# Kernel optimization log

Measured on AMD Instinct MI355X. Metric: run time of the kernel, lower is better.

## Reference

```python
import jax, jax.numpy as jnp
import numpy as np

B, T, H, L, AS = 64, 256, 1024, 3, 128  # batch, seq-1, hidden, layers, alphabet


def setup_inputs() -> dict:
    key = jax.random.key(0)
    ks = jax.random.split(key, 8)
    # one-hot character sequence (B, T, AS), float32
    idx = jax.random.randint(ks[0], (B, T), 0, AS)
    sequence = jax.nn.one_hot(idx, AS, dtype=jnp.float32)
    u = lambda k, shape, fan: jax.random.uniform(
        k, shape, minval=-1.0 / np.sqrt(fan), maxval=1.0 / np.sqrt(fan), dtype=jnp.float32)
    W_i2h = u(ks[1], (H, AS), AS)
    b_i2h = u(ks[2], (H,), AS)
    # per-layer LSTM params, PyTorch gate order [i, f, g, o]; layer inputs all have width H
    W_ih = u(ks[3], (L, 4 * H, H), H)
    W_hh = u(ks[4], (L, 4 * H, H), H)
    b_ih = u(ks[5], (L, 4 * H), H)
    b_hh = u(ks[6], (L, 4 * H), H)
    W_h2O = u(ks[7], (AS, H), H)
    b_h2O = jnp.zeros((AS,), dtype=jnp.float32)
    h0 = jnp.zeros((L, B, H), dtype=jnp.float32)
    c0 = jnp.zeros((L, B, H), dtype=jnp.float32)
    return dict(sequence=sequence, W_i2h=W_i2h, b_i2h=b_i2h, W_ih=W_ih, W_hh=W_hh,
                b_ih=b_ih, b_hh=b_hh, W_h2O=W_h2O, b_h2O=b_h2O, h0=h0, c0=c0)


def _lstm_layer(x, h0, c0, W_ih, W_hh, b_ih, b_hh):
    # x: (B, T, H). Precompute input contribution to the gates for all steps.
    xg = jnp.einsum('bth,gh->btg', x, W_ih) + b_ih  # (B, T, 4H)

    def step(carry, xg_t):
        h, c = carry
        gates = xg_t + h @ W_hh.T + b_hh  # (B, 4H)
        i, f, g, o = jnp.split(gates, 4, axis=-1)
        c = jax.nn.sigmoid(f) * c + jax.nn.sigmoid(i) * jnp.tanh(g)
        h = jax.nn.sigmoid(o) * jnp.tanh(c)
        return (h, c), h

    (hT, cT), hs = jax.lax.scan(step, (h0, c0), jnp.swapaxes(xg, 0, 1))
    return jnp.swapaxes(hs, 0, 1), hT, cT  # (B,T,H), (B,H), (B,H)


def reference(sequence, W_i2h, b_i2h, W_ih, W_hh, b_ih, b_hh, W_h2O, b_h2O, h0, c0):
    # i2h projection
    x = jnp.einsum('bta,ha->bth', sequence, W_i2h) + b_i2h  # (B, T, H)
    # multi-layer LSTM over x (eval mode: the dropout=True arg is inactive in eval)
    inp = x
    h_fin, c_fin = [], []
    for l in range(L):
        inp, hT, cT = _lstm_layer(inp, h0[l], c0[l], W_ih[l], W_hh[l], b_ih[l], b_hh[l])
        h_fin.append(hT)
        c_fin.append(cT)
    # NOTE: faithful to the original code's bug -- h2O is applied to the i2h
    # output `x`, not to the LSTM output. The LSTM only produces the new hidden.
    out = x.reshape(-1, H) @ W_h2O.T + b_h2O  # (B*T, AS)
    return out, jnp.stack(h_fin), jnp.stack(c_fin)
```

## Files before the change

### kernel.cpp

```cpp
#include <hip/hip_runtime.h>
#include <stdint.h>
#include <stddef.h>

#define B_  64
#define T_  256
#define H_  1024
#define AS_ 128
#define L_  3

typedef __attribute__((ext_vector_type(8))) short bf16x8;
typedef __attribute__((ext_vector_type(4))) float f32x4;
typedef __attribute__((ext_vector_type(4))) unsigned u32x4;

__device__ __forceinline__ unsigned short f2bf(float f) {
  union { float f; unsigned u; } x; x.f = f;
  unsigned r = x.u + 0x7fffu + ((x.u >> 16) & 1u);
  return (unsigned short)(r >> 16);
}
__device__ __forceinline__ float bf2f(unsigned short s) {
  union { unsigned u; float f; } x; x.u = ((unsigned)s) << 16; return x.f;
}
__device__ __forceinline__ float sigmf(float x) { return 1.0f / (1.0f + __expf(-x)); }
__device__ __forceinline__ float tanh_f(float x) {
  x = fminf(fmaxf(x, -15.0f), 15.0f);
  float e = __expf(2.0f * x);
  return (e - 1.0f) / (e + 1.0f);
}

__device__ __forceinline__ void st_u16_cc(unsigned short* p, unsigned short v) {
  __hip_atomic_store(p, v, __ATOMIC_RELAXED, __HIP_MEMORY_SCOPE_AGENT);
}
__device__ __forceinline__ void st_u32_cc(unsigned* p, unsigned v) {
  __hip_atomic_store(p, v, __ATOMIC_RELAXED, __HIP_MEMORY_SCOPE_AGENT);
}
__device__ __forceinline__ unsigned ld_u32_cc(const unsigned* p) {
  return __hip_atomic_load(p, __ATOMIC_RELAXED, __HIP_MEMORY_SCOPE_AGENT);
}
__device__ __forceinline__ u32x4 ld_b128_cc_nw(const void* p) {
  u32x4 r;
  asm volatile("global_load_dwordx4 %0, %1, off sc0 sc1" : "=v"(r) : "v"(p));
  return r;
}
__device__ __forceinline__ void wait_vm4_tie4(u32x4& a, u32x4& b, u32x4& c, u32x4& d) {
  asm volatile("s_waitcnt vmcnt(4)"
               : "+v"(a), "+v"(b), "+v"(c), "+v"(d) :: "memory");
  __builtin_amdgcn_sched_barrier(0);
}
__device__ __forceinline__ void wait_vm0_tie4(u32x4& a, u32x4& b, u32x4& c, u32x4& d) {
  asm volatile("s_waitcnt vmcnt(0)"
               : "+v"(a), "+v"(b), "+v"(c), "+v"(d) :: "memory");
  __builtin_amdgcn_sched_barrier(0);
}
__device__ __forceinline__ void lds_barrier() {
  __builtin_amdgcn_sched_barrier(0);
  asm volatile("s_waitcnt lgkmcnt(0)" ::: "memory");
  __builtin_amdgcn_sched_barrier(0);
  __builtin_amdgcn_s_barrier();
  __builtin_amdgcn_sched_barrier(0);
}


__global__ void k_zero(unsigned* p, int n) {
  int i = blockIdx.x * 256 + threadIdx.x;
  if (i < n) st_u32_cc(p + i, 0u);
}

__global__ void k_wt_i2h(const float* __restrict__ W, const float* __restrict__ b,
                         unsigned short* __restrict__ Wt) {
  int id = blockIdx.x * 256 + threadIdx.x;
  if (id >= AS_ * H_) return;
  int a = id >> 10, h = id & 1023;
  Wt[id] = f2bf(W[h * AS_ + a] + b[h]);
}

__global__ void k_f2b(const float* __restrict__ s, unsigned short* __restrict__ d, int n) {
  int i = blockIdx.x * 256 + threadIdx.x;
  if (i < n) d[i] = f2bf(s[i]);
}

__global__ void k_bias(const float* __restrict__ bi, const float* __restrict__ bh,
                       float* __restrict__ o, int n) {
  int i = blockIdx.x * 256 + threadIdx.x;
  if (i < n) o[i] = bi[i] + bh[i];
}

__global__ __launch_bounds__(128) void k_gather(const float* __restrict__ seq,
                                                const unsigned short* __restrict__ Wt,
                                                unsigned short* __restrict__ xbf) {
  __shared__ int sidx;
  const int bt = blockIdx.x, tid = threadIdx.x;
  if (seq[(size_t)bt * AS_ + tid] > 0.5f) sidx = tid;
  __syncthreads();
  const uint4* s = (const uint4*)(Wt + (size_t)sidx * H_);
  uint4* d = (uint4*)(xbf + (size_t)bt * H_);
  d[tid] = s[tid];
}


__device__ __forceinline__ void gld16(const void* g, void* l) {
  __builtin_amdgcn_global_load_lds((const __attribute__((address_space(1))) unsigned int*)g,
                                   (__attribute__((address_space(3))) unsigned int*)l,
                                   16, 0, 0);
}

template <int OUT>
__global__ __launch_bounds__(256) void k_gemm(const unsigned short* __restrict__ A,
                                              const unsigned short* __restrict__ Bm,
                                              const float* __restrict__ bias,
                                              void* __restrict__ Cout,
                                              int M, int N, int K) {
  __shared__ __align__(16) unsigned short As[128 * 32];
  __shared__ __align__(16) unsigned short Bs[128 * 32];
  const int tid = threadIdx.x, lane = tid & 63, wv = tid >> 6;
  const int m0 = blockIdx.x * 128, n0 = blockIdx.y * 128;
  const int wr = wv >> 1, wc = wv & 1;
  const int kg = lane >> 4, li = lane & 15;
  f32x4 acc[4][4] = {};

  for (int k0 = 0; k0 < K; k0 += 32) {
    for (int i = 0; i < 2; ++i) {
      int c0 = i * 256 + wv * 64;
      int cid = c0 + lane;
      int row = cid >> 2, lc = cid & 3;
      int sc = lc ^ ((row >> 1) & 3);
      gld16(A + (size_t)(m0 + row) * K + k0 + sc * 8, (char*)As + (size_t)c0 * 16);
      gld16(Bm + (size_t)(n0 + row) * K + k0 + sc * 8, (char*)Bs + (size_t)c0 * 16);
    }
    __syncthreads();
    bf16x8 af[4], bfm[4];
#pragma unroll
    for (int mi = 0; mi < 4; ++mi) {
      int row = wr * 64 + mi * 16 + li;
      int pc = kg ^ ((row >> 1) & 3);
      af[mi] = *(const bf16x8*)((const char*)As + row * 64 + pc * 16);
    }
#pragma unroll
    for (int ni = 0; ni < 4; ++ni) {
      int row = wc * 64 + ni * 16 + li;
      int pc = kg ^ ((row >> 1) & 3);
      bfm[ni] = *(const bf16x8*)((const char*)Bs + row * 64 + pc * 16);
    }
#pragma unroll
    for (int mi = 0; mi < 4; ++mi)
#pragma unroll
      for (int ni = 0; ni < 4; ++ni)
        acc[mi][ni] = __builtin_amdgcn_mfma_f32_16x16x32_bf16(af[mi], bfm[ni], acc[mi][ni], 0, 0, 0);
    __syncthreads();
  }

#pragma unroll
  for (int mi = 0; mi < 4; ++mi)
#pragma unroll
    for (int ni = 0; ni < 4; ++ni)
#pragma unroll
      for (int r = 0; r < 4; ++r) {
        int row = m0 + wr * 64 + mi * 16 + kg * 4 + r;
        int col = n0 + wc * 64 + ni * 16 + li;
        float v = acc[mi][ni][r] + bias[col];
        if (OUT == 0) {
          ((float*)Cout)[(size_t)row * N + col] = v;
        } else {
          int b = row >> 8, tt = row & 255;
          int g = col >> 10, u = col & 1023;
          int idx = ((tt * 4 + (b >> 4)) << 16) | ((u >> 5) << 11) |
                    ((b & 15) << 7) | ((u & 31) << 2) | g;
          ((unsigned short*)Cout)[idx] = f2bf(v);
        }
      }
}


__global__ __launch_bounds__(256, 1) void k_scan(
    const unsigned short* __restrict__ xgs,
    const float* __restrict__ Whh,
    unsigned short* __restrict__ h_pp,
    unsigned short* __restrict__ out_seq,
    float* __restrict__ hT, float* __restrict__ cT,
    const float* __restrict__ h0, const float* __restrict__ c0,
    unsigned* __restrict__ slots) {
  __shared__ __align__(16) unsigned short Wlds[64 * 1024];
  __shared__ __align__(16) unsigned short Hs[16 * 1024];
  const int tid = threadIdx.x, lane = tid & 63, w = tid >> 6;
  const int gb = blockIdx.x >> 5, ug = blockIdx.x & 31;
  const int li = lane & 15, kq = lane >> 4;
  const int b  = gb * 16 + li;
  const int u0 = ug * 32 + w * 8 + kq;
  const int u1 = u0 + 4;

  st_u16_cc(&h_pp[((size_t)B_ + b) * H_ + u0], f2bf(h0[(size_t)b * H_ + u0]));
  st_u16_cc(&h_pp[((size_t)B_ + b) * H_ + u1], f2bf(h0[(size_t)b * H_ + u1]));

  bf16x8 afr[32];
  {
    const int r0 = w * 32 + li;
    const float* wr = Whh + ((size_t)(r0 & 3) * H_ + ug * 32 + (r0 >> 2)) * H_ + kq * 8;
#pragma unroll
    for (int ks = 0; ks < 32; ++ks) {
      const float4 f0 = *(const float4*)(wr + ks * 32);
      const float4 f1 = *(const float4*)(wr + ks * 32 + 4);
      union { ushort4 a[2]; bf16x8 v; } uu_;
      uu_.a[0] = ushort4{f2bf(f0.x), f2bf(f0.y), f2bf(f0.z), f2bf(f0.w)};
      uu_.a[1] = ushort4{f2bf(f1.x), f2bf(f1.y), f2bf(f1.z), f2bf(f1.w)};
      afr[ks] = uu_.v;
    }
  }
  for (int it = 0; it < 16; ++it) {
    const int r = w * 32 + 16 + it;
    const float* wr = Whh + ((size_t)(r & 3) * H_ + ug * 32 + (r >> 2)) * H_;
#pragma unroll
    for (int j = 0; j < 4; ++j) {
      const float4 f = *(const float4*)(wr + lane * 16 + j * 4);
      ushort4 p = ushort4{f2bf(f.x), f2bf(f.y), f2bf(f.z), f2bf(f.w)};
      const int k = lane * 16 + j * 4;
      *(ushort4*)((char*)Wlds + (size_t)(w * 16 + it) * 2048 + ((2 * k) ^ ((it & 7) << 4))) = p;
    }
  }
  float cs0 = c0[(size_t)b * H_ + u0], cs1 = c0[(size_t)b * H_ + u1];
  __syncthreads();
  if (w == 3 && lane < 32) {
    st_u32_cc(&slots[gb * 1024 + lane * 32 + ug], 1u);
    asm volatile("s_waitcnt vmcnt(0)" ::: "memory");
  }

  const char* hbase = (const char*)Hs + (size_t)li * 2048;
  const char* wlb   = (const char*)Wlds + (size_t)(w * 16 + li) * 2048;
  const int fxor = (li & 7) << 4;
  const int sb = tid >> 4, seg = tid & 15;
  const int sswz = (sb & 7) << 4;
  char* drow = (char*)Hs + (size_t)sb * 2048;
  unsigned short* exch = Hs;
  const unsigned* myline = slots + gb * 1024 + ug * 32;

  for (int t = 0; t < T_; ++t) {
    const size_t xb2 = ((((size_t)t * 4 + gb) << 16) | (ug << 11) | (li << 7) |
                        ((w * 8 + kq) << 2)) * 2;
    const ushort4 xa = *(const ushort4*)((const char*)xgs + xb2);
    const ushort4 xb = *(const ushort4*)((const char*)xgs + xb2 + 32);

    if (w == 0) {
      const unsigned tgt = (unsigned)(t + 1);
      unsigned v;
      do {
        __builtin_amdgcn_s_sleep(1);
        v = ld_u32_cc(&myline[lane & 31]);
      } while (__any((int)(v < tgt)));
    }
    __syncthreads();

    const char* srcrow = (const char*)(h_pp + (size_t)((t & 1) ^ 1) * (B_ * H_) +
                                       (size_t)(gb * 16 + sb) * H_);
    u32x4 A0 = ld_b128_cc_nw(srcrow +   0 * 256 + seg * 16);
    u32x4 A1 = ld_b128_cc_nw(srcrow +   1 * 256 + seg * 16);
    u32x4 A2 = ld_b128_cc_nw(srcrow +   2 * 256 + seg * 16);
    u32x4 A3 = ld_b128_cc_nw(srcrow +   3 * 256 + seg * 16);
    u32x4 B0 = ld_b128_cc_nw(srcrow + 1024 + 0 * 256 + seg * 16);
    u32x4 B1 = ld_b128_cc_nw(srcrow + 1024 + 1 * 256 + seg * 16);
    u32x4 B2 = ld_b128_cc_nw(srcrow + 1024 + 2 * 256 + seg * 16);
    u32x4 B3 = ld_b128_cc_nw(srcrow + 1024 + 3 * 256 + seg * 16);
    wait_vm4_tie4(A0, A1, A2, A3);
    *(u32x4*)(drow + ((0 * 256 + seg * 16) ^ sswz)) = A0;
    *(u32x4*)(drow + ((1 * 256 + seg * 16) ^ sswz)) = A1;
    *(u32x4*)(drow + ((2 * 256 + seg * 16) ^ sswz)) = A2;
    *(u32x4*)(drow + ((3 * 256 + seg * 16) ^ sswz)) = A3;
    lds_barrier();

    f32x4 a0 = {0.f, 0.f, 0.f, 0.f}, a1 = {0.f, 0.f, 0.f, 0.f};
#pragma unroll
    for (int ks = 0; ks < 16; ++ks) {
      const bf16x8 bb = *(const bf16x8*)(hbase + ((ks * 64 + kq * 16) ^ fxor));
      a0 = __builtin_amdgcn_mfma_f32_16x16x32_bf16(afr[ks], bb, a0, 0, 0, 0);
      const bf16x8 aw = *(const bf16x8*)(wlb + ((ks * 64 + kq * 16) ^ fxor));
      a1 = __builtin_amdgcn_mfma_f32_16x16x32_bf16(aw, bb, a1, 0, 0, 0);
    }

    wait_vm0_tie4(B0, B1, B2, B3);
    *(u32x4*)(drow + ((1024 + 0 * 256 + seg * 16) ^ sswz)) = B0;
    *(u32x4*)(drow + ((1024 + 1 * 256 + seg * 16) ^ sswz)) = B1;
    *(u32x4*)(drow + ((1024 + 2 * 256 + seg * 16) ^ sswz)) = B2;
    *(u32x4*)(drow + ((1024 + 3 * 256 + seg * 16) ^ sswz)) = B3;
    lds_barrier();

#pragma unroll
    for (int ks = 16; ks < 32; ++ks) {
      const bf16x8 bb = *(const bf16x8*)(hbase + ((ks * 64 + kq * 16) ^ fxor));
      a0 = __builtin_amdgcn_mfma_f32_16x16x32_bf16(afr[ks], bb, a0, 0, 0, 0);
      const bf16x8 aw = *(const bf16x8*)(wlb + ((ks * 64 + kq * 16) ^ fxor));
      a1 = __builtin_amdgcn_mfma_f32_16x16x32_bf16(aw, bb, a1, 0, 0, 0);
    }

    float h0v, h1v;
    {
      float gi = a0[0] + bf2f(xa.x), gf = a0[1] + bf2f(xa.y);
      float gg = a0[2] + bf2f(xa.z), go = a0[3] + bf2f(xa.w);
      float ci = sigmf(gf) * cs0 + sigmf(gi) * tanh_f(gg);
      cs0 = ci; h0v = sigmf(go) * tanh_f(ci);
    }
    {
      float gi = a1[0] + bf2f(xb.x), gf = a1[1] + bf2f(xb.y);
      float gg = a1[2] + bf2f(xb.z), go = a1[3] + bf2f(xb.w);
      float ci = sigmf(gf) * cs1 + sigmf(gi) * tanh_f(gg);
      cs1 = ci; h1v = sigmf(go) * tanh_f(ci);
    }
    const unsigned short hb0 = f2bf(h0v), hb1 = f2bf(h1v);

    __syncthreads();
    exch[li * 32 + w * 8 + kq]     = hb0;
    exch[li * 32 + w * 8 + kq + 4] = hb1;
    __syncthreads();

    if (t < T_ - 1) {
      const int bl = tid >> 4, j = tid & 15;
      const unsigned pack = (unsigned)exch[bl * 32 + 2 * j] |
                            ((unsigned)exch[bl * 32 + 2 * j + 1] << 16);
      st_u32_cc((unsigned*)&h_pp[((size_t)(t & 1) * B_ + gb * 16 + bl) * H_ + ug * 32 + 2 * j],
                pack);
      asm volatile("s_waitcnt vmcnt(0)" ::: "memory");
      __syncthreads();
      if (w == 3 && lane < 32) {
        st_u32_cc(&slots[gb * 1024 + lane * 32 + ug], (unsigned)(t + 2));
        asm volatile("s_waitcnt vmcnt(0)" ::: "memory");
      }
    } else {
      hT[(size_t)b * H_ + u0] = h0v; hT[(size_t)b * H_ + u1] = h1v;
      cT[(size_t)b * H_ + u0] = cs0; cT[(size_t)b * H_ + u1] = cs1;
    }

    if (out_seq && tid < 64) {
      const int bo = tid >> 2, q = tid & 3;
      *(u32x4*)&out_seq[((size_t)(gb * 16 + bo) * T_ + t) * H_ + ug * 32 + 8 * q] =
          *(const u32x4*)&exch[bo * 32 + 8 * q];
    }
  }
}


extern "C" void kernel_launch(void* const* d_in, const int* in_sizes, int n_in,
                              void* d_out, int out_size, void* d_ws, size_t ws_size,
                              hipStream_t stream) {
  const float* seq  = (const float*)d_in[0];
  const float* Wi2h = (const float*)d_in[1];
  const float* bi2h = (const float*)d_in[2];
  const float* Wih  = (const float*)d_in[3];
  const float* Whh  = (const float*)d_in[4];
  const float* bih  = (const float*)d_in[5];
  const float* bhh  = (const float*)d_in[6];
  const float* Wh2o = (const float*)d_in[7];
  const float* bh2o = (const float*)d_in[8];
  const float* h0   = (const float*)d_in[9];
  const float* c0   = (const float*)d_in[10];
  float* outF = (float*)d_out;

  size_t off = 0;
  auto nb = [&](size_t bytes) { size_t r = off; off += (bytes + 255) & ~(size_t)255; return r; };
  unsigned short* xbf   = (unsigned short*)((char*)d_ws + nb((size_t)B_ * T_ * H_ * 2));
  unsigned short* seqA  = (unsigned short*)((char*)d_ws + nb((size_t)B_ * T_ * H_ * 2));
  unsigned short* xgs   = (unsigned short*)((char*)d_ws + nb((size_t)B_ * T_ * 4 * H_ * 2));
  unsigned short* Wihb  = (unsigned short*)((char*)d_ws + nb((size_t)L_ * 4 * H_ * H_ * 2));
  unsigned short* Wh2ob = (unsigned short*)((char*)d_ws + nb((size_t)AS_ * H_ * 2));
  unsigned short* Wt    = (unsigned short*)((char*)d_ws + nb((size_t)AS_ * H_ * 2));
  float*          bsum  = (float*)((char*)d_ws + nb((size_t)L_ * 4 * H_ * 4));
  unsigned short* h_pp  = (unsigned short*)((char*)d_ws + nb((size_t)2 * B_ * H_ * 2));
  unsigned*       slt   = (unsigned*)((char*)d_ws + nb((size_t)L_ * 4 * 32 * 32 * 4));
  (void)ws_size; (void)in_sizes; (void)n_in; (void)out_size;

  const int WLAYER = 4 * H_ * H_;

  k_zero<<<(L_ * 4096 + 255) / 256, 256, 0, stream>>>(slt, L_ * 4096);
  k_wt_i2h<<<(AS_ * H_ + 255) / 256, 256, 0, stream>>>(Wi2h, bi2h, Wt);
  k_f2b<<<(L_ * WLAYER + 255) / 256, 256, 0, stream>>>(Wih, Wihb, L_ * WLAYER);
  k_f2b<<<(AS_ * H_ + 255) / 256, 256, 0, stream>>>(Wh2o, Wh2ob, AS_ * H_);
  k_bias<<<(L_ * 4 * H_ + 255) / 256, 256, 0, stream>>>(bih, bhh, bsum, L_ * 4 * H_);
  k_gather<<<B_ * T_, 128, 0, stream>>>(seq, Wt, xbf);

  k_gemm<0><<<dim3(B_ * T_ / 128, AS_ / 128), 256, 0, stream>>>(
      xbf, Wh2ob, bh2o, (void*)outF, B_ * T_, AS_, H_);

  float* hT_base = outF + (size_t)B_ * T_ * AS_;
  float* cT_base = hT_base + (size_t)L_ * B_ * H_;

  for (int l = 0; l < L_; ++l) {
    const unsigned short* Ain = (l == 0) ? xbf : (l == 1) ? seqA : xbf;
    unsigned short* oseq = (l == 0) ? seqA : (l == 1) ? xbf : nullptr;
    k_gemm<2><<<dim3(B_ * T_ / 128, 4 * H_ / 128), 256, 0, stream>>>(
        Ain, Wihb + (size_t)l * WLAYER, bsum + (size_t)l * 4 * H_, (void*)xgs,
        B_ * T_, 4 * H_, H_);
    k_scan<<<128, 256, 0, stream>>>(
        xgs, Whh + (size_t)l * WLAYER, h_pp, oseq,
        hT_base + (size_t)l * B_ * H_, cT_base + (size_t)l * B_ * H_,
        h0 + (size_t)l * B_ * H_, c0 + (size_t)l * B_ * H_,
        slt + (size_t)l * 4096);
  }
}
```

Measured before the change: 3.696 ms.

## Overlap next layer's input GEMM with the LSTM scan in one fused kernel

```diff
diff --git a/kernel.cpp b/kernel.cpp
--- a/kernel.cpp
+++ b/kernel.cpp
@@ -40,6 +40,9 @@
   u32x4 r;
   asm volatile("global_load_dwordx4 %0, %1, off sc0 sc1" : "=v"(r) : "v"(p));
   return r;
+}
+__device__ __forceinline__ void st_b128_cc_nw(void* p, u32x4 v) {
+  asm volatile("global_store_dwordx4 %0, %1, off sc0 sc1" :: "v"(p), "v"(v) : "memory");
 }
 __device__ __forceinline__ void wait_vm4_tie4(u32x4& a, u32x4& b, u32x4& c, u32x4& d) {
   asm volatile("s_waitcnt vmcnt(4)"
@@ -103,16 +106,14 @@
                                    16, 0, 0);
 }
 
-template <int OUT>
-__global__ __launch_bounds__(256) void k_gemm(const unsigned short* __restrict__ A,
-                                              const unsigned short* __restrict__ Bm,
-                                              const float* __restrict__ bias,
-                                              void* __restrict__ Cout,
-                                              int M, int N, int K) {
-  __shared__ __align__(16) unsigned short As[128 * 32];
-  __shared__ __align__(16) unsigned short Bs[128 * 32];
-  const int tid = threadIdx.x, lane = tid & 63, wv = tid >> 6;
-  const int m0 = blockIdx.x * 128, n0 = blockIdx.y * 128;
+template <int OUT, int AMAJ>
+__device__ __forceinline__ void gemm_tile(const unsigned short* __restrict__ A,
+                                          const unsigned short* __restrict__ Bm,
+                                          const float* __restrict__ bias,
+                                          void* __restrict__ Cout,
+                                          int m0, int n0, int K, int N, int tid,
+                                          unsigned short* As, unsigned short* Bs) {
+  const int lane = tid & 63, wv = tid >> 6;
   const int wr = wv >> 1, wc = wv & 1;
   const int kg = lane >> 4, li = lane & 15;
   f32x4 acc[4][4] = {};
@@ -160,7 +161,9 @@
         if (OUT == 0) {
           ((float*)Cout)[(size_t)row * N + col] = v;
         } else {
-          int b = row >> 8, tt = row & 255;
+          int b, tt;
+          if (AMAJ == 0) { b = row >> 8; tt = row & 255; }
+          else           { tt = row >> 6; b = row & 63; }
           int g = col >> 10, u = col & 1023;
           int idx = ((tt * 4 + (b >> 4)) << 16) | ((u >> 5) << 11) |
                     ((b & 15) << 7) | ((u & 31) << 2) | g;
@@ -169,19 +172,61 @@
       }
 }
 
-
-__global__ __launch_bounds__(256, 1) void k_scan(
+template <int OUT, int AMAJ>
+__global__ __launch_bounds__(256) void k_gemm(const unsigned short* __restrict__ A,
+                                              const unsigned short* __restrict__ Bm,
+                                              const float* __restrict__ bias,
+                                              void* __restrict__ Cout,
+                                              int M, int N, int K) {
+  __shared__ __align__(16) unsigned short As[128 * 32];
+  __shared__ __align__(16) unsigned short Bs[128 * 32];
+  gemm_tile<OUT, AMAJ>(A, Bm, bias, Cout, blockIdx.x * 128, blockIdx.y * 128,
+                       K, N, threadIdx.x, As, Bs);
+}
+
+
+__global__ __launch_bounds__(256, 1) void k_fused(
     const unsigned short* __restrict__ xgs,
     const float* __restrict__ Whh,
     unsigned short* __restrict__ h_pp,
     unsigned short* __restrict__ out_seq,
     float* __restrict__ hT, float* __restrict__ cT,
     const float* __restrict__ h0, const float* __restrict__ c0,
-    unsigned* __restrict__ slots) {
+    unsigned* __restrict__ slots,
+    const unsigned short* __restrict__ WihbN,
+    const float* __restrict__ bsumN,
+    unsigned short* __restrict__ xgs_out) {
   __shared__ __align__(16) unsigned short Wlds[64 * 1024];
   __shared__ __align__(16) unsigned short Hs[16 * 1024];
   const int tid = threadIdx.x, lane = tid & 63, w = tid >> 6;
-  const int gb = blockIdx.x >> 5, ug = blockIdx.x & 31;
+  const int wg = blockIdx.x;
+
+  if (wg >= 128) {
+    const int Wp = wg - 128;
+    unsigned short* As = Wlds;
+    unsigned short* Bs = Wlds + 4096;
+    const int pline = (Wp & 31) * 32;
+    for (int k = 0; k < 32; ++k) {
+      const int gidx = Wp + k * 128;
+      const int mt = gidx >> 5, nt = gidx & 31;
+      const unsigned tgt = (unsigned)(2 * mt + 3);
+      if (w == 0) {
+        const unsigned* base = slots + (lane >> 4) * 1024 + pline + (lane & 15);
+        unsigned v0, v1;
+        do {
+          __builtin_amdgcn_s_sleep(4);
+          v0 = ld_u32_cc(base);
+          v1 = ld_u32_cc(base + 16);
+        } while (__any((int)((v0 < tgt) | (v1 < tgt))));
+      }
+      __syncthreads();
+      gemm_tile<2, 1>(out_seq, WihbN, bsumN, (void*)xgs_out,
+                      mt * 128, nt * 128, H_, 4 * H_, tid, As, Bs);
+    }
+    return;
+  }
+
+  const int gb = wg >> 5, ug = wg & 31;
   const int li = lane & 15, kq = lane >> 4;
   const int b  = gb * 16 + li;
   const int u0 = ug * 32 + w * 8 + kq;
@@ -314,21 +359,20 @@
                             ((unsigned)exch[bl * 32 + 2 * j + 1] << 16);
       st_u32_cc((unsigned*)&h_pp[((size_t)(t & 1) * B_ + gb * 16 + bl) * H_ + ug * 32 + 2 * j],
                 pack);
-      asm volatile("s_waitcnt vmcnt(0)" ::: "memory");
-      __syncthreads();
-      if (w == 3 && lane < 32) {
-        st_u32_cc(&slots[gb * 1024 + lane * 32 + ug], (unsigned)(t + 2));
-        asm volatile("s_waitcnt vmcnt(0)" ::: "memory");
-      }
     } else {
       hT[(size_t)b * H_ + u0] = h0v; hT[(size_t)b * H_ + u1] = h1v;
       cT[(size_t)b * H_ + u0] = cs0; cT[(size_t)b * H_ + u1] = cs1;
     }
-
     if (out_seq && tid < 64) {
       const int bo = tid >> 2, q = tid & 3;
-      *(u32x4*)&out_seq[((size_t)(gb * 16 + bo) * T_ + t) * H_ + ug * 32 + 8 * q] =
-          *(const u32x4*)&exch[bo * 32 + 8 * q];
+      st_b128_cc_nw(&out_seq[((size_t)t * B_ + gb * 16 + bo) * H_ + ug * 32 + 8 * q],
+                    *(const u32x4*)&exch[bo * 32 + 8 * q]);
+    }
+    asm volatile("s_waitcnt vmcnt(0)" ::: "memory");
+    __syncthreads();
+    if (w == 3 && lane < 32) {
+      st_u32_cc(&slots[gb * 1024 + lane * 32 + ug], (unsigned)(t + 2));
+      asm volatile("s_waitcnt vmcnt(0)" ::: "memory");
     }
   }
 }
@@ -372,22 +416,29 @@
   k_bias<<<(L_ * 4 * H_ + 255) / 256, 256, 0, stream>>>(bih, bhh, bsum, L_ * 4 * H_);
   k_gather<<<B_ * T_, 128, 0, stream>>>(seq, Wt, xbf);
 
-  k_gemm<0><<<dim3(B_ * T_ / 128, AS_ / 128), 256, 0, stream>>>(
+  k_gemm<0, 0><<<dim3(B_ * T_ / 128, AS_ / 128), 256, 0, stream>>>(
       xbf, Wh2ob, bh2o, (void*)outF, B_ * T_, AS_, H_);
+
+  k_gemm<2, 0><<<dim3(B_ * T_ / 128, 4 * H_ / 128), 256, 0, stream>>>(
+      xbf, Wihb, bsum, (void*)xgs, B_ * T_, 4 * H_, H_);
 
   float* hT_base = outF + (size_t)B_ * T_ * AS_;
   float* cT_base = hT_base + (size_t)L_ * B_ * H_;
 
-  for (int l = 0; l < L_; ++l) {
-    const unsigned short* Ain = (l == 0) ? xbf : (l == 1) ? seqA : xbf;
-    unsigned short* oseq = (l == 0) ? seqA : (l == 1) ? xbf : nullptr;
-    k_gemm<2><<<dim3(B_ * T_ / 128, 4 * H_ / 128), 256, 0, stream>>>(
-        Ain, Wihb + (size_t)l * WLAYER, bsum + (size_t)l * 4 * H_, (void*)xgs,
-        B_ * T_, 4 * H_, H_);
-    k_scan<<<128, 256, 0, stream>>>(
-        xgs, Whh + (size_t)l * WLAYER, h_pp, oseq,
-        hT_base + (size_t)l * B_ * H_, cT_base + (size_t)l * B_ * H_,
-        h0 + (size_t)l * B_ * H_, c0 + (size_t)l * B_ * H_,
-        slt + (size_t)l * 4096);
-  }
-}
+  k_fused<<<256, 256, 0, stream>>>(
+      xgs, Whh, h_pp, seqA,
+      hT_base, cT_base, h0, c0, slt,
+      Wihb + (size_t)1 * WLAYER, bsum + (size_t)1 * 4 * H_, xgs);
+
+  k_fused<<<256, 256, 0, stream>>>(
+      xgs, Whh + (size_t)1 * WLAYER, h_pp, xbf,
+      hT_base + (size_t)B_ * H_, cT_base + (size_t)B_ * H_,
+      h0 + (size_t)B_ * H_, c0 + (size_t)B_ * H_, slt + (size_t)4096,
+      Wihb + (size_t)2 * WLAYER, bsum + (size_t)2 * 4 * H_, xgs);
+
+  k_fused<<<128, 256, 0, stream>>>(
+      xgs, Whh + (size_t)2 * WLAYER, h_pp, nullptr,
+      hT_base + (size_t)2 * B_ * H_, cT_base + (size_t)2 * B_ * H_,
+      h0 + (size_t)2 * B_ * H_, c0 + (size_t)2 * B_ * H_, slt + (size_t)2 * 4096,
+      nullptr, nullptr, nullptr);
+}
```

Result: faster. 3.488 ms (-5.6%).
